# Optimization experiments

Measured on AMD Instinct MI355X. Metric: run time of the kernel, lower is better.

Reference implementation:

```python
import jax, jax.numpy as jnp
import numpy as np

N = 50000          # num nodes
E = 800000         # num edges (avg degree 16)
C_IN = 64          # input channels
TOWERS = 4
F_IN = C_IN // TOWERS       # 16 (divide_input=True)
OUT = 128
F_OUT = OUT // TOWERS       # 32
NUM_AGG = 4                 # mean, std, max, min
NUM_SC = 3                  # identity, amplification, attenuation
AVG_LOG_DEG = float(np.log(17.0))  # deg histogram: all nodes degree 16 -> log(16+1)


def setup_inputs() -> dict:
    key = jax.random.key(0)
    ks = jax.random.split(key, 10)
    nodes = jax.random.normal(ks[0], (N, C_IN), dtype=jnp.float32)
    senders = jax.random.randint(ks[1], (E,), 0, N)
    receivers = jax.random.randint(ks[2], (E,), 0, N)
    # per-tower pre-MLP: Linear(2*F_IN -> F_IN), pre_layers=1 (no activation)
    pre_w = jax.random.normal(ks[3], (TOWERS, 2 * F_IN, F_IN), dtype=jnp.float32) / np.sqrt(2 * F_IN)
    pre_b = jnp.zeros((TOWERS, F_IN), dtype=jnp.float32)
    # per-tower post-MLP: Linear(F_IN + F_IN*12 -> F_OUT), post_layers=1
    post_in = F_IN + F_IN * NUM_AGG * NUM_SC  # 208
    post_w = jax.random.normal(ks[4], (TOWERS, post_in, F_OUT), dtype=jnp.float32) / np.sqrt(post_in)
    post_b = jnp.zeros((TOWERS, F_OUT), dtype=jnp.float32)
    # final linear: TOWERS*F_OUT -> OUT
    lin_w = jax.random.normal(ks[5], (TOWERS * F_OUT, OUT), dtype=jnp.float32) / np.sqrt(TOWERS * F_OUT)
    lin_b = jnp.zeros((OUT,), dtype=jnp.float32)
    return {"nodes": nodes, "senders": senders, "receivers": receivers,
            "pre_w": pre_w, "pre_b": pre_b, "post_w": post_w, "post_b": post_b,
            "lin_w": lin_w, "lin_b": lin_b}


def reference(nodes, senders, receivers, pre_w, pre_b, post_w, post_b, lin_w, lin_b):
    # divide_input=True: split channels across towers -> [N, T, F_IN]
    x = nodes.reshape(N, TOWERS, F_IN)
    x_i = x[senders]                                  # [E, T, F_IN]
    x_j = x[receivers]                                # [E, T, F_IN]
    h = jnp.concatenate([x_i, x_j], axis=-1)          # [E, T, 2*F_IN]
    # per-tower pre-MLP (single linear), vectorized over towers
    msg = jnp.einsum('etf,tfo->eto', h, pre_w) + pre_b  # [E, T, F_IN]

    # degree-scaled multi-aggregator segment reduce over receivers
    count = jax.ops.segment_sum(jnp.ones((E,), dtype=msg.dtype), receivers, num_segments=N)  # [N]
    d = jnp.clip(count, 1.0, None)
    inv_d = (1.0 / d)[:, None, None]
    mean = jax.ops.segment_sum(msg, receivers, num_segments=N) * inv_d           # [N,T,F]
    mean_sq = jax.ops.segment_sum(msg * msg, receivers, num_segments=N) * inv_d
    std = jnp.sqrt(jax.nn.relu(mean_sq - mean * mean) + 1e-5)
    has_nb = (count > 0)[:, None, None]
    mx = jax.ops.segment_max(msg, receivers, num_segments=N)
    mx = jnp.where(has_nb, mx, 0.0)
    mn = -jax.ops.segment_max(-msg, receivers, num_segments=N)
    mn = jnp.where(has_nb, mn, 0.0)
    agg = jnp.concatenate([mean, std, mx, mn], axis=-1)  # [N, T, 4*F_IN]

    # scalers: identity, amplification, attenuation (degree clamped to >= 1)
    log_d = jnp.log(d + 1.0)[:, None, None]
    amp = log_d / AVG_LOG_DEG
    att = AVG_LOG_DEG / log_d
    scaled = jnp.concatenate([agg, agg * amp, agg * att], axis=-1)  # [N, T, 12*F_IN]

    out = jnp.concatenate([x, scaled], axis=-1)                     # [N, T, 13*F_IN]
    outs = jnp.einsum('ntf,tfo->nto', out, post_w) + post_b         # [N, T, F_OUT]
    flat = outs.reshape(N, TOWERS * F_OUT)                          # [N, 128]
    return flat @ lin_w + lin_b                                     # [N, OUT]
```

## Files before the change

### kernel.cpp

```cpp
#include <hip/hip_runtime.h>

#define AVG_LOG_DEG 2.8332133440562162f
#define CAP 64
#define CSTRIDE 16

typedef __attribute__((ext_vector_type(8))) short short8;
typedef __attribute__((ext_vector_type(4))) float f32x4;

static __device__ __forceinline__ float bl(unsigned u) { return __uint_as_float(u << 16); }
static __device__ __forceinline__ float bh(unsigned u) { return __uint_as_float(u & 0xffff0000u); }
static __device__ __forceinline__ unsigned short f2b(float f) {
    unsigned u = __float_as_uint(f);
    return (unsigned short)((u + 0x7fffu + ((u >> 16) & 1u)) >> 16);
}
static __device__ __forceinline__ unsigned pk(unsigned short lo, unsigned short hi) {
    return (unsigned)lo | ((unsigned)hi << 16);
}


__global__ __launch_bounds__(256) void k_setup(
    const float* __restrict__ nodes, const float* __restrict__ pre_w,
    const float* __restrict__ pre_b,
    const float* __restrict__ post_w, const float* __restrict__ lin_w,
    unsigned short* __restrict__ Yh, float* __restrict__ H,
    unsigned short* __restrict__ postT,
    unsigned short* __restrict__ linT, int* __restrict__ cursor,
    int n, int A, int nZ)
{
    int b = blockIdx.x;
    if (b < A) {
        int lane = threadIdx.x & 63;
        int wid = threadIdx.x >> 6;
        int t = lane >> 4, f = lane & 15;
        float w0[16], w1[16];
        #pragma unroll
        for (int k = 0; k < 16; ++k) {
            w0[k] = pre_w[(t * 32 + k) * 16 + f];
            w1[k] = pre_w[(t * 32 + 16 + k) * 16 + f];
        }
        float hb = pre_b[t * 16 + f];
        int nbase = b * 64 + wid * 16;
        for (int jj = 0; jj < 16; ++jj) {
            int node = nbase + jj;
            if (node >= n) break;
            const float4* xp = reinterpret_cast<const float4*>(nodes + (size_t)node * 64 + t * 16);
            float4 x0 = xp[0], x1 = xp[1], x2 = xp[2], x3 = xp[3];
            float xs[16] = {x0.x, x0.y, x0.z, x0.w, x1.x, x1.y, x1.z, x1.w,
                            x2.x, x2.y, x2.z, x2.w, x3.x, x3.y, x3.z, x3.w};
            float y = 0.f;
            float h = hb;
            #pragma unroll
            for (int k = 0; k < 16; ++k) {
                y = fmaf(xs[k], w0[k], y);
                h = fmaf(xs[k], w1[k], h);
            }
            Yh[(size_t)node * 64 + lane] = f2b(y);
            H[(size_t)node * 64 + lane] = h;
        }
    } else if (b < A + 176) {
        int i = (b - A) * 256 + threadIdx.x;
        if (i < 28672) {
            int t = i / (32 * 224);
            int r = i % (32 * 224);
            int nn = r / 224;
            int k = r % 224;
            float wv;
            if (k < 192)      wv = post_w[((size_t)t * 208 + 16 + k) * 32 + nn];
            else if (k < 208) wv = post_w[((size_t)t * 208 + (k - 192)) * 32 + nn];
            else              wv = 0.f;
            postT[i] = f2b(wv);
        }
        int j = i - 28672;
        if (j >= 0 && j < 16384) {
            int nn = j >> 7, k = j & 127;
            linT[j] = f2b(lin_w[k * 128 + nn]);
        }
    } else {
        int i = (b - A - 176) * 1024 + threadIdx.x * 4;
        if (i < nZ) {
            int4 z; z.x = z.y = z.z = z.w = 0;
            *reinterpret_cast<int4*>(cursor + i) = z;
        }
    }
}


__global__ __launch_bounds__(256) void k_bin(
    const int* __restrict__ send, const int* __restrict__ recv,
    int* __restrict__ bktCnt, int2* __restrict__ bktArr,
    int e, int eCap)
{
    __shared__ int2 stage[2048];
    __shared__ int wcnt[4][8], wbase[4][8], btot[8], bbase[8], pref[9];

    int tid = threadIdx.x;
    int lane = tid & 63, wid = tid >> 6;
    int base = blockIdx.x * 2048 + wid * 512 + lane;

    int rv[8], sv[8], rk[8];
    unsigned long long lt = (1ULL << lane) - 1ULL;
    unsigned long long runLo = 0, runHi = 0;

    #pragma unroll
    for (int q = 0; q < 8; ++q) {
        int idx = base + q * 64;
        bool valid = idx < e;
        rv[q] = valid ? recv[idx] : 0;
        sv[q] = valid ? send[idx] : 0;
        int bb = rv[q] & 7;
        unsigned long long m0 = __ballot(bb & 1);
        unsigned long long m1 = __ballot(bb & 2);
        unsigned long long m2 = __ballot(bb & 4);
        unsigned long long mv = __ballot(valid);
        unsigned long long mo = ((bb & 1) ? m0 : ~m0) & ((bb & 2) ? m1 : ~m1)
                              & ((bb & 4) ? m2 : ~m2) & mv;
        unsigned long long sel = (bb & 4) ? runHi : runLo;
        int runb = (int)((sel >> ((bb & 3) * 16)) & 0xffffULL);
        rk[q] = runb + __popcll(mo & lt);
        unsigned long long addLo = 0, addHi = 0;
        #pragma unroll
        for (int k = 0; k < 4; ++k) {
            unsigned long long mkl = ((k & 1) ? m0 : ~m0) & ((k & 2) ? m1 : ~m1) & ~m2 & mv;
            unsigned long long mkh = ((k & 1) ? m0 : ~m0) & ((k & 2) ? m1 : ~m1) &  m2 & mv;
            addLo |= (unsigned long long)__popcll(mkl) << (k * 16);
            addHi |= (unsigned long long)__popcll(mkh) << (k * 16);
        }
        runLo += addLo; runHi += addHi;
        if (!valid) rk[q] = -1;
    }
    if (lane < 8) {
        unsigned long long sel = (lane & 4) ? runHi : runLo;
        wcnt[wid][lane] = (int)((sel >> ((lane & 3) * 16)) & 0xffffULL);
    }
    __syncthreads();
    if (tid < 8) {
        int c0 = wcnt[0][tid], c1 = wcnt[1][tid], c2 = wcnt[2][tid], c3 = wcnt[3][tid];
        wbase[0][tid] = 0;
        wbase[1][tid] = c0;
        wbase[2][tid] = c0 + c1;
        wbase[3][tid] = c0 + c1 + c2;
        int bt = c0 + c1 + c2 + c3;
        btot[tid] = bt;
        bbase[tid] = atomicAdd(&bktCnt[tid], bt);
    }
    __syncthreads();
    if (tid == 0) {
        int acc = 0;
        #pragma unroll
        for (int k = 0; k < 8; ++k) { pref[k] = acc; acc += btot[k]; }
        pref[8] = acc;
    }
    __syncthreads();
    #pragma unroll
    for (int q = 0; q < 8; ++q) {
        if (rk[q] >= 0) {
            int bb = rv[q] & 7;
            int pos = pref[bb] + wbase[wid][bb] + rk[q];
            int2 ed; ed.x = rv[q]; ed.y = sv[q];
            stage[pos] = ed;
        }
    }
    __syncthreads();
    int tot = pref[8];
    for (int i = tid; i < tot; i += 256) {
        int k = 0;
        #pragma unroll
        for (int j = 1; j < 8; ++j) k += (i >= pref[j]);
        int g = bbase[k] + (i - pref[k]);
        if (g < eCap)
            bktArr[(size_t)k * eCap + g] = stage[i];
    }
}


__global__ __launch_bounds__(256) void k_scatter2(
    const int* __restrict__ bktCnt, const int2* __restrict__ bktArr,
    int* __restrict__ cursor, int* __restrict__ slots, int eCap)
{
    int bkt = blockIdx.x & 7;
    int cnt = min(bktCnt[bkt], eCap);
    const int2* ba = bktArr + (size_t)bkt * eCap;
    for (int i = (blockIdx.x >> 3) * 256 + threadIdx.x; i < cnt; i += 256 * 256) {
        int2 ed = ba[i];
        int p = atomicAdd(&cursor[(size_t)ed.x * CSTRIDE], 1);
        if (p < CAP) slots[(size_t)ed.x * CAP + p] = ed.y;
    }
}


__global__ __launch_bounds__(256) void k_agg(
    const int* __restrict__ cursor,
    const int* __restrict__ slots,
    const unsigned short* __restrict__ Yh,
    const float* __restrict__ H,
    unsigned short* __restrict__ aggh, int n)
{
    int lane = threadIdx.x & 63;
    int node = blockIdx.x * 4 + (threadIdx.x >> 6);
    if (node >= n) return;
    int t = lane >> 4, f = lane & 15;

    int idxv = slots[(size_t)node * CAP + lane];
    float hjw = H[(size_t)node * 64 + lane];
    int d = min(cursor[(size_t)node * CSTRIDE], CAP);
    const unsigned short* Yl = Yh + lane;

    float s = 0.f, s2 = 0.f, mx = -INFINITY, mn = INFINITY;
    int e = 0;
    for (; e + 16 <= d; e += 16) {
        unsigned v[16];
        #pragma unroll
        for (int q = 0; q < 16; ++q) {
            int si = __builtin_amdgcn_readlane(idxv, e + q);
            v[q] = Yl[(size_t)si * 64];
        }
        #pragma unroll
        for (int q = 0; q < 16; ++q) {
            float m = __uint_as_float(v[q] << 16) + hjw;
            s += m;
            s2 = fmaf(m, m, s2);
            mx = fmaxf(mx, m);
            mn = fminf(mn, m);
        }
    }
    int rem = d - e;
    if (rem > 0) {
        unsigned v[16];
        #pragma unroll
        for (int q = 0; q < 16; ++q) {
            int si = __builtin_amdgcn_readlane(idxv, min(e + q, d - 1));
            v[q] = Yl[(size_t)si * 64];
        }
        #pragma unroll
        for (int q = 0; q < 16; ++q) {
            if (q < rem) {
                float m = __uint_as_float(v[q] << 16) + hjw;
                s += m;
                s2 = fmaf(m, m, s2);
                mx = fmaxf(mx, m);
                mn = fminf(mn, m);
            }
        }
    }

    float dc = fmaxf((float)d, 1.f);
    float inv = 1.f / dc;
    float mean = s * inv;
    float var = fmaf(-mean, mean, s2 * inv);
    float sd = sqrtf(fmaxf(var, 0.f) + 1e-5f);
    if (d == 0) { mx = 0.f; mn = 0.f; }

    unsigned short* ag = aggh + (size_t)node * 256 + t * 64 + f;
    ag[0]  = f2b(mean);
    ag[16] = f2b(sd);
    ag[32] = f2b(mx);
    ag[48] = f2b(mn);
}


__global__ __launch_bounds__(256, 3) void k_post(
    const float* __restrict__ nodes,
    const unsigned short* __restrict__ aggh,
    const int* __restrict__ deg,
    const unsigned short* __restrict__ postT,
    const unsigned short* __restrict__ linT,
    const float* __restrict__ post_b,
    const float* __restrict__ lin_b,
    float* __restrict__ out, int n)
{
    __shared__ unsigned short sV[32 * 256];
    __shared__ unsigned short sFlat[32 * 128];
    __shared__ float sAmp[32], sAtt[32];

    int tid = threadIdx.x;
    int n0 = blockIdx.x * 32;

    if (tid < 32) {
        int g = min(n0 + tid, n - 1);
        float dc = fmaxf((float)min(deg[(size_t)g * CSTRIDE], CAP), 1.f);
        float ld = logf(dc + 1.f);
        sAmp[tid] = ld * (1.f / AVG_LOG_DEG);
        sAtt[tid] = AVG_LOG_DEG / ld;
    }

    int w = tid >> 6, lane = tid & 63;
    int quad = lane >> 4, mr = lane & 15;
    int mstrip = w & 1, nhalf = w >> 1;
    int nn = tid >> 3, j8 = tid & 7;
    int sw = nn & 7;
    int gn = min(n0 + nn, n - 1);
    int rsw = mr & 7;

    uint4 pa4[4];
    #pragma unroll
    for (int t = 0; t < 4; ++t)
        pa4[t] = *reinterpret_cast<const uint4*>(aggh + (size_t)gn * 256 + t * 64 + j8 * 8);

    uint4 xw4[4];
    #pragma unroll
    for (int t = 0; t < 4; ++t) { xw4[t].x = 0; xw4[t].y = 0; xw4[t].z = 0; xw4[t].w = 0; }
    if (j8 < 2) {
        #pragma unroll
        for (int t = 0; t < 4; ++t) {
            const float4* xp = reinterpret_cast<const float4*>(nodes + (size_t)gn * 64 + t * 16 + j8 * 8);
            float4 xa = xp[0], xb = xp[1];
            xw4[t].x = pk(f2b(xa.x), f2b(xa.y)); xw4[t].y = pk(f2b(xa.z), f2b(xa.w));
            xw4[t].z = pk(f2b(xb.x), f2b(xb.y)); xw4[t].w = pk(f2b(xb.z), f2b(xb.w));
        }
    }

    const unsigned short* bbase = postT + (size_t)(nhalf * 16 + mr) * 224 + quad * 8;
    short8 bA[7], bB[7];
    #pragma unroll
    for (int kk = 0; kk < 7; ++kk) bA[kk] = *reinterpret_cast<const short8*>(bbase + kk * 32);
    #pragma unroll
    for (int kk = 0; kk < 7; ++kk) bB[kk] = *reinterpret_cast<const short8*>(bbase + 32 * 224 + kk * 32);

    __syncthreads();
    float ampv = sAmp[nn], attv = sAtt[nn];

    #pragma unroll
    for (int t = 0; t < 4; ++t) {
        {
            unsigned short* row = &sV[nn * 256];
            uint4 a = pa4[t];
            *reinterpret_cast<uint4*>(row + (j8 ^ sw) * 8) = a;
            unsigned uu[4] = {a.x, a.y, a.z, a.w};
            unsigned short pa[8], pb[8];
            #pragma unroll
            for (int q = 0; q < 4; ++q) {
                float lo = bl(uu[q]), hi = bh(uu[q]);
                pa[2*q]   = f2b(lo * ampv); pa[2*q+1] = f2b(hi * ampv);
                pb[2*q]   = f2b(lo * attv); pb[2*q+1] = f2b(hi * attv);
            }
            uint4 wa, wb;
            wa.x = pk(pa[0], pa[1]); wa.y = pk(pa[2], pa[3]);
            wa.z = pk(pa[4], pa[5]); wa.w = pk(pa[6], pa[7]);
            wb.x = pk(pb[0], pb[1]); wb.y = pk(pb[2], pb[3]);
            wb.z = pk(pb[4], pb[5]); wb.w = pk(pb[6], pb[7]);
            *reinterpret_cast<uint4*>(row + (8  + (j8 ^ sw)) * 8) = wa;
            *reinterpret_cast<uint4*>(row + (16 + (j8 ^ sw)) * 8) = wb;
            *reinterpret_cast<uint4*>(row + (24 + (j8 ^ sw)) * 8) = xw4[t];
        }
        __syncthreads();

        f32x4 acc = {0.f, 0.f, 0.f, 0.f};
        const unsigned short* av0 = &sV[(mstrip * 16 + mr) * 256];
        #pragma unroll
        for (int kk = 0; kk < 7; ++kk) {
            int c = kk * 4 + quad;
            int pc = (c & ~7) | ((c & 7) ^ rsw);
            short8 avv = *reinterpret_cast<const short8*>(av0 + pc * 8);
            if (t & 1) acc = __builtin_amdgcn_mfma_f32_16x16x32_bf16(avv, bB[kk], acc, 0, 0, 0);
            else       acc = __builtin_amdgcn_mfma_f32_16x16x32_bf16(avv, bA[kk], acc, 0, 0, 0);
        }

        if (t == 0) {
            #pragma unroll
            for (int kk = 0; kk < 7; ++kk)
                bA[kk] = *reinterpret_cast<const short8*>(bbase + 2 * 32 * 224 + kk * 32);
        } else if (t == 1) {
            #pragma unroll
            for (int kk = 0; kk < 7; ++kk)
                bB[kk] = *reinterpret_cast<const short8*>(bbase + 3 * 32 * 224 + kk * 32);
        }

        int col = t * 32 + nhalf * 16 + mr;
        float pbv = post_b[col];
        int cc = col >> 3, co = col & 7;
        #pragma unroll
        for (int i = 0; i < 4; ++i) {
            int rowf = mstrip * 16 + quad * 4 + i;
            int pc = (cc & ~7) | ((cc & 7) ^ (rowf & 7));
            sFlat[rowf * 128 + pc * 8 + co] = f2b(acc[i] + pbv);
        }
        __syncthreads();
    }

    f32x4 facc[4];
    #pragma unroll
    for (int nt = 0; nt < 4; ++nt) { facc[nt].x = 0.f; facc[nt].y = 0.f; facc[nt].z = 0.f; facc[nt].w = 0.f; }

    const unsigned short* af0 = &sFlat[(mstrip * 16 + mr) * 128];
    #pragma unroll
    for (int kk = 0; kk < 4; ++kk) {
        int c = kk * 4 + quad;
        int pc = (c & ~7) | ((c & 7) ^ rsw);
        short8 avv = *reinterpret_cast<const short8*>(af0 + pc * 8);
        #pragma unroll
        for (int nt = 0; nt < 4; ++nt) {
            short8 bv = *reinterpret_cast<const short8*>(
                linT + (size_t)(nhalf * 64 + nt * 16 + mr) * 128 + kk * 32 + quad * 8);
            facc[nt] = __builtin_amdgcn_mfma_f32_16x16x32_bf16(avv, bv, facc[nt], 0, 0, 0);
        }
    }

    #pragma unroll
    for (int nt = 0; nt < 4; ++nt) {
        int col = nhalf * 64 + nt * 16 + mr;
        float lb = lin_b[col];
        #pragma unroll
        for (int i = 0; i < 4; ++i) {
            int node = n0 + mstrip * 16 + quad * 4 + i;
            if (node < n) out[(size_t)node * 128 + col] = facc[nt][i] + lb;
        }
    }
}

extern "C" void kernel_launch(void* const* d_in, const int* in_sizes, int n_in,
                              void* d_out, int out_size, void* d_ws, size_t ws_size,
                              hipStream_t stream)
{
    const float* nodes  = (const float*)d_in[0];
    const int*   send   = (const int*)d_in[1];
    const int*   recv   = (const int*)d_in[2];
    const float* pre_w  = (const float*)d_in[3];
    const float* pre_b  = (const float*)d_in[4];
    const float* post_w = (const float*)d_in[5];
    const float* post_b = (const float*)d_in[6];
    const float* lin_w  = (const float*)d_in[7];
    const float* lin_b  = (const float*)d_in[8];
    float* out = (float*)d_out;

    int N = in_sizes[0] / 64;
    int E = in_sizes[1];
    int Npad = (N + 255) & ~255;

    int* cursor = (int*)d_ws;
    int* bktCnt = cursor + (size_t)Npad * CSTRIDE;
    int2* bktArr = (int2*)(bktCnt + 256);
    int* slots  = (int*)(bktArr + (size_t)8 * E);
    unsigned short* Yh = (unsigned short*)(slots + (size_t)Npad * CAP);
    float* H = (float*)(Yh + (size_t)Npad * 64);
    unsigned short* aggh  = (unsigned short*)(H + (size_t)Npad * 64);
    unsigned short* postT = aggh + (size_t)Npad * 256;
    unsigned short* linT  = postT + 28672;

    int nZ = Npad * CSTRIDE + 256;
    int nbZ = (nZ + 1023) / 1024;
    int A = (N + 63) / 64;
    int nbBin = (E + 2047) / 2048;

    k_setup   <<<A + 176 + nbZ, 256, 0, stream>>>(nodes, pre_w, pre_b, post_w, lin_w,
                                                  Yh, H, postT, linT, cursor, N, A, nZ);
    k_bin     <<<nbBin, 256, 0, stream>>>(send, recv, bktCnt, bktArr, E, E);
    k_scatter2<<<2048, 256, 0, stream>>>(bktCnt, bktArr, cursor, slots, E);
    k_agg     <<<(N + 3) / 4, 256, 0, stream>>>(cursor, slots, Yh, H, aggh, N);
    k_post    <<<(N + 31) / 32, 256, 0, stream>>>(nodes, aggh, cursor, postT, linT,
                                                  post_b, lin_b, out, N);
}
```

Before: 205.0 us.

## Fuse edge binning into setup kernel with per-block bucket segments

The edge-binning kernel is merged into the setup launch as extra blocks. Each bin block now writes its bucket counts and edges into fixed per-block segments instead of taking global atomic offsets into shared buckets. The scatter pass walks those segments per bucket. The node pre-MLP blocks are also split four times finer (16 nodes per block), which removes one launch and the global bucket-counter atomics but adds more setup blocks and a per-segment loop in scatter.

```diff
diff --git a/kernel.cpp b/kernel.cpp
--- a/kernel.cpp
+++ b/kernel.cpp
@@ -22,15 +22,20 @@
     const float* __restrict__ nodes, const float* __restrict__ pre_w,
     const float* __restrict__ pre_b,
     const float* __restrict__ post_w, const float* __restrict__ lin_w,
+    const int* __restrict__ send, const int* __restrict__ recv,
     unsigned short* __restrict__ Yh, float* __restrict__ H,
-    unsigned short* __restrict__ postT,
-    unsigned short* __restrict__ linT, int* __restrict__ cursor,
-    int n, int A, int nZ)
+    unsigned short* __restrict__ postT, unsigned short* __restrict__ linT,
+    int* __restrict__ cursor, int* __restrict__ wcntG, int2* __restrict__ bktArr,
+    int n, int A, int nZ, int nbZ, int e)
 {
+    __shared__ int2 stage[2048];
+    __shared__ int wcnt[4][8], btot[8], pref[9];
+
     int b = blockIdx.x;
+    int tid = threadIdx.x;
     if (b < A) {
-        int lane = threadIdx.x & 63;
-        int wid = threadIdx.x >> 6;
+        int lane = tid & 63;
+        int wid = tid >> 6;
         int t = lane >> 4, f = lane & 15;
         float w0[16], w1[16];
         #pragma unroll
@@ -39,8 +44,9 @@
             w1[k] = pre_w[(t * 32 + 16 + k) * 16 + f];
         }
         float hb = pre_b[t * 16 + f];
-        int nbase = b * 64 + wid * 16;
-        for (int jj = 0; jj < 16; ++jj) {
+        int nbase = b * 16 + wid * 4;
+        #pragma unroll
+        for (int jj = 0; jj < 4; ++jj) {
             int node = nbase + jj;
             if (node >= n) break;
             const float4* xp = reinterpret_cast<const float4*>(nodes + (size_t)node * 64 + t * 16);
@@ -58,7 +64,7 @@
             H[(size_t)node * 64 + lane] = h;
         }
     } else if (b < A + 176) {
-        int i = (b - A) * 256 + threadIdx.x;
+        int i = (b - A) * 256 + tid;
         if (i < 28672) {
             int t = i / (32 * 224);
             int r = i % (32 * 224);
@@ -75,115 +81,108 @@
             int nn = j >> 7, k = j & 127;
             linT[j] = f2b(lin_w[k * 128 + nn]);
         }
-    } else {
-        int i = (b - A - 176) * 1024 + threadIdx.x * 4;
+    } else if (b < A + 176 + nbZ) {
+        int i = (b - A - 176) * 1024 + tid * 4;
         if (i < nZ) {
             int4 z; z.x = z.y = z.z = z.w = 0;
             *reinterpret_cast<int4*>(cursor + i) = z;
         }
-    }
-}
-
-
-__global__ __launch_bounds__(256) void k_bin(
-    const int* __restrict__ send, const int* __restrict__ recv,
-    int* __restrict__ bktCnt, int2* __restrict__ bktArr,
-    int e, int eCap)
-{
-    __shared__ int2 stage[2048];
-    __shared__ int wcnt[4][8], wbase[4][8], btot[8], bbase[8], pref[9];
-
-    int tid = threadIdx.x;
-    int lane = tid & 63, wid = tid >> 6;
-    int base = blockIdx.x * 2048 + wid * 512 + lane;
-
-    int rv[8], sv[8], rk[8];
-    unsigned long long lt = (1ULL << lane) - 1ULL;
-    unsigned long long runLo = 0, runHi = 0;
-
-    #pragma unroll
-    for (int q = 0; q < 8; ++q) {
-        int idx = base + q * 64;
-        bool valid = idx < e;
-        rv[q] = valid ? recv[idx] : 0;
-        sv[q] = valid ? send[idx] : 0;
-        int bb = rv[q] & 7;
-        unsigned long long m0 = __ballot(bb & 1);
-        unsigned long long m1 = __ballot(bb & 2);
-        unsigned long long m2 = __ballot(bb & 4);
-        unsigned long long mv = __ballot(valid);
-        unsigned long long mo = ((bb & 1) ? m0 : ~m0) & ((bb & 2) ? m1 : ~m1)
-                              & ((bb & 4) ? m2 : ~m2) & mv;
-        unsigned long long sel = (bb & 4) ? runHi : runLo;
-        int runb = (int)((sel >> ((bb & 3) * 16)) & 0xffffULL);
-        rk[q] = runb + __popcll(mo & lt);
-        unsigned long long addLo = 0, addHi = 0;
-        #pragma unroll
-        for (int k = 0; k < 4; ++k) {
-            unsigned long long mkl = ((k & 1) ? m0 : ~m0) & ((k & 2) ? m1 : ~m1) & ~m2 & mv;
-            unsigned long long mkh = ((k & 1) ? m0 : ~m0) & ((k & 2) ? m1 : ~m1) &  m2 & mv;
-            addLo |= (unsigned long long)__popcll(mkl) << (k * 16);
-            addHi |= (unsigned long long)__popcll(mkh) << (k * 16);
-        }
-        runLo += addLo; runHi += addHi;
-        if (!valid) rk[q] = -1;
-    }
-    if (lane < 8) {
-        unsigned long long sel = (lane & 4) ? runHi : runLo;
-        wcnt[wid][lane] = (int)((sel >> ((lane & 3) * 16)) & 0xffffULL);
-    }
-    __syncthreads();
-    if (tid < 8) {
-        int c0 = wcnt[0][tid], c1 = wcnt[1][tid], c2 = wcnt[2][tid], c3 = wcnt[3][tid];
-        wbase[0][tid] = 0;
-        wbase[1][tid] = c0;
-        wbase[2][tid] = c0 + c1;
-        wbase[3][tid] = c0 + c1 + c2;
-        int bt = c0 + c1 + c2 + c3;
-        btot[tid] = bt;
-        bbase[tid] = atomicAdd(&bktCnt[tid], bt);
-    }
-    __syncthreads();
-    if (tid == 0) {
-        int acc = 0;
-        #pragma unroll
-        for (int k = 0; k < 8; ++k) { pref[k] = acc; acc += btot[k]; }
-        pref[8] = acc;
-    }
-    __syncthreads();
-    #pragma unroll
-    for (int q = 0; q < 8; ++q) {
-        if (rk[q] >= 0) {
-            int bb = rv[q] & 7;
-            int pos = pref[bb] + wbase[wid][bb] + rk[q];
-            int2 ed; ed.x = rv[q]; ed.y = sv[q];
-            stage[pos] = ed;
-        }
-    }
-    __syncthreads();
-    int tot = pref[8];
-    for (int i = tid; i < tot; i += 256) {
-        int k = 0;
-        #pragma unroll
-        for (int j = 1; j < 8; ++j) k += (i >= pref[j]);
-        int g = bbase[k] + (i - pref[k]);
-        if (g < eCap)
-            bktArr[(size_t)k * eCap + g] = stage[i];
+    } else {
+        int bb = b - A - 176 - nbZ;
+        int lane = tid & 63, wid = tid >> 6;
+        int base = bb * 2048 + wid * 512 + lane;
+
+        int rv[8], sv[8], rk[8];
+        unsigned long long lt = (1ULL << lane) - 1ULL;
+        unsigned long long runLo = 0, runHi = 0;
+
+        #pragma unroll
+        for (int q = 0; q < 8; ++q) {
+            int idx = base + q * 64;
+            bool valid = idx < e;
+            rv[q] = valid ? recv[idx] : 0;
+            sv[q] = valid ? send[idx] : 0;
+            int bkb = rv[q] & 7;
+            unsigned long long m0 = __ballot(bkb & 1);
+            unsigned long long m1 = __ballot(bkb & 2);
+            unsigned long long m2 = __ballot(bkb & 4);
+            unsigned long long mv = __ballot(valid);
+            unsigned long long mo = ((bkb & 1) ? m0 : ~m0) & ((bkb & 2) ? m1 : ~m1)
+                                  & ((bkb & 4) ? m2 : ~m2) & mv;
+            unsigned long long sel = (bkb & 4) ? runHi : runLo;
+            int runb = (int)((sel >> ((bkb & 3) * 16)) & 0xffffULL);
+            rk[q] = runb + __popcll(mo & lt);
+            unsigned long long addLo = 0, addHi = 0;
+            #pragma unroll
+            for (int k = 0; k < 4; ++k) {
+                unsigned long long mkl = ((k & 1) ? m0 : ~m0) & ((k & 2) ? m1 : ~m1) & ~m2 & mv;
+                unsigned long long mkh = ((k & 1) ? m0 : ~m0) & ((k & 2) ? m1 : ~m1) &  m2 & mv;
+                addLo |= (unsigned long long)__popcll(mkl) << (k * 16);
+                addHi |= (unsigned long long)__popcll(mkh) << (k * 16);
+            }
+            runLo += addLo; runHi += addHi;
+            if (!valid) rk[q] = -1;
+        }
+        if (lane < 8) {
+            unsigned long long sel = (lane & 4) ? runHi : runLo;
+            wcnt[wid][lane] = (int)((sel >> ((lane & 3) * 16)) & 0xffffULL);
+        }
+        __syncthreads();
+        if (tid < 8) {
+            int c0 = wcnt[0][tid], c1 = wcnt[1][tid], c2 = wcnt[2][tid], c3 = wcnt[3][tid];
+            wcnt[0][tid] = 0;
+            wcnt[1][tid] = c0;
+            wcnt[2][tid] = c0 + c1;
+            wcnt[3][tid] = c0 + c1 + c2;
+            int bt = c0 + c1 + c2 + c3;
+            btot[tid] = bt;
+            wcntG[bb * 8 + tid] = bt;
+        }
+        __syncthreads();
+        if (tid == 0) {
+            int acc = 0;
+            #pragma unroll
+            for (int k = 0; k < 8; ++k) { pref[k] = acc; acc += btot[k]; }
+            pref[8] = acc;
+        }
+        __syncthreads();
+        #pragma unroll
+        for (int q = 0; q < 8; ++q) {
+            if (rk[q] >= 0) {
+                int bkb = rv[q] & 7;
+                int pos = pref[bkb] + wcnt[wid][bkb] + rk[q];
+                int2 ed; ed.x = rv[q]; ed.y = sv[q];
+                stage[pos] = ed;
+            }
+        }
+        __syncthreads();
+        int tot = pref[8];
+        for (int i = tid; i < tot; i += 256) {
+            int k = 0;
+            #pragma unroll
+            for (int j = 1; j < 8; ++j) k += (i >= pref[j]);
+            int g = i - pref[k];
+            if (g < 2048)
+                bktArr[((size_t)bb * 8 + k) * 2048 + g] = stage[i];
+        }
     }
 }
 
 
 __global__ __launch_bounds__(256) void k_scatter2(
-    const int* __restrict__ bktCnt, const int2* __restrict__ bktArr,
-    int* __restrict__ cursor, int* __restrict__ slots, int eCap)
+    const int* __restrict__ wcntG, const int2* __restrict__ bktArr,
+    int* __restrict__ cursor, int* __restrict__ slots, int nseg)
 {
     int bkt = blockIdx.x & 7;
-    int cnt = min(bktCnt[bkt], eCap);
-    const int2* ba = bktArr + (size_t)bkt * eCap;
-    for (int i = (blockIdx.x >> 3) * 256 + threadIdx.x; i < cnt; i += 256 * 256) {
-        int2 ed = ba[i];
-        int p = atomicAdd(&cursor[(size_t)ed.x * CSTRIDE], 1);
-        if (p < CAP) slots[(size_t)ed.x * CAP + p] = ed.y;
+    int grp = blockIdx.x >> 3;
+    for (int s = grp; s < nseg; s += 256) {
+        int cnt = min(wcntG[s * 8 + bkt], 2048);
+        const int2* ba = bktArr + ((size_t)s * 8 + bkt) * 2048;
+        for (int i = threadIdx.x; i < cnt; i += 256) {
+            int2 ed = ba[i];
+            int p = atomicAdd(&cursor[(size_t)ed.x * CSTRIDE], 1);
+            if (p < CAP) slots[(size_t)ed.x * CAP + p] = ed.y;
+        }
     }
 }
 
@@ -425,26 +424,26 @@
     int N = in_sizes[0] / 64;
     int E = in_sizes[1];
     int Npad = (N + 255) & ~255;
+    int nbBin = (E + 2047) / 2048;
 
     int* cursor = (int*)d_ws;
-    int* bktCnt = cursor + (size_t)Npad * CSTRIDE;
-    int2* bktArr = (int2*)(bktCnt + 256);
-    int* slots  = (int*)(bktArr + (size_t)8 * E);
+    int* wcntG  = cursor + (size_t)Npad * CSTRIDE;
+    int2* bktArr = (int2*)(wcntG + (size_t)nbBin * 8);
+    int* slots  = (int*)(bktArr + (size_t)nbBin * 8 * 2048);
     unsigned short* Yh = (unsigned short*)(slots + (size_t)Npad * CAP);
     float* H = (float*)(Yh + (size_t)Npad * 64);
     unsigned short* aggh  = (unsigned short*)(H + (size_t)Npad * 64);
     unsigned short* postT = aggh + (size_t)Npad * 256;
     unsigned short* linT  = postT + 28672;
 
-    int nZ = Npad * CSTRIDE + 256;
+    int nZ = Npad * CSTRIDE;
     int nbZ = (nZ + 1023) / 1024;
-    int A = (N + 63) / 64;
-    int nbBin = (E + 2047) / 2048;
-
-    k_setup   <<<A + 176 + nbZ, 256, 0, stream>>>(nodes, pre_w, pre_b, post_w, lin_w,
-                                                  Yh, H, postT, linT, cursor, N, A, nZ);
-    k_bin     <<<nbBin, 256, 0, stream>>>(send, recv, bktCnt, bktArr, E, E);
-    k_scatter2<<<2048, 256, 0, stream>>>(bktCnt, bktArr, cursor, slots, E);
+    int A = (N + 15) / 16;
+
+    k_setup   <<<A + 176 + nbZ + nbBin, 256, 0, stream>>>(
+        nodes, pre_w, pre_b, post_w, lin_w, send, recv,
+        Yh, H, postT, linT, cursor, wcntG, bktArr, N, A, nZ, nbZ, E);
+    k_scatter2<<<2048, 256, 0, stream>>>(wcntG, bktArr, cursor, slots, nbBin);
     k_agg     <<<(N + 3) / 4, 256, 0, stream>>>(cursor, slots, Yh, H, aggh, N);
     k_post    <<<(N + 31) / 32, 256, 0, stream>>>(nodes, aggh, cursor, postT, linT,
                                                   post_b, lin_b, out, N);
```

Result: faster. 200.0 us (-2.4%).
